# Optimization experiments

Hardware: AMD Instinct MI355X
Metric: run time of the kernel (lower is better)

## Reference

```python
import jax, jax.numpy as jnp
import numpy as np

SEQ, BATCH, HIDDEN = 2048, 2, 1024
NUM_HEADS, HEAD_DIM = 16, 64
LN_EPS = 1e-6
NEG_INF = -1e10


def setup_inputs() -> dict:
    key = jax.random.key(0)
    k1, k2, k3, k4 = jax.random.split(key, 4)
    inputs_q = jax.random.normal(k1, (SEQ, BATCH, HIDDEN), dtype=jnp.float32)
    # mask convention (TE flax): True / 1 => position is masked out
    mask = jax.random.randint(k2, (BATCH, 1, SEQ, SEQ), 0, 2).astype(bool)
    ln_scale = jnp.ones((HIDDEN,), dtype=jnp.float32)
    ln_bias = jnp.zeros((HIDDEN,), dtype=jnp.float32)
    # fused QKV kernel (embed, 3, num_heads*head_dim); query column pre-scaled
    # at init by 1/sqrt(head_dim) (scaled_query_init=True)
    w_qkv = jax.random.normal(k3, (HIDDEN, 3, NUM_HEADS * HEAD_DIM), dtype=jnp.float32) / np.sqrt(HIDDEN)
    w_qkv = w_qkv.at[:, 0, :].divide(np.sqrt(HEAD_DIM))
    w_out = jax.random.normal(k4, (NUM_HEADS * HEAD_DIM, HIDDEN), dtype=jnp.float32) / np.sqrt(NUM_HEADS * HEAD_DIM)
    return {"inputs_q": inputs_q, "mask": mask, "ln_scale": ln_scale,
            "ln_bias": ln_bias, "w_qkv": w_qkv, "w_out": w_out}


def _layernorm(x, scale, bias):
    mean = jnp.mean(x, axis=-1, keepdims=True)
    var = jnp.mean(jnp.square(x - mean), axis=-1, keepdims=True)
    return (x - mean) * jax.lax.rsqrt(var + LN_EPS) * scale + bias


def reference(inputs_q, mask, ln_scale, ln_bias, w_qkv, w_out):
    s, b, e = inputs_q.shape  # (seq, batch, hidden): transpose_batch_sequence=True
    ln_out = _layernorm(inputs_q, ln_scale, ln_bias)
    # fused QKV projection: (s,b,e) @ (e,3,H*D) -> (s,b,3,H*D)
    qkv = jnp.einsum('sbe,ekf->sbkf', ln_out, w_qkv)
    q, k, v = qkv[:, :, 0, :], qkv[:, :, 1, :], qkv[:, :, 2, :]
    q = q.reshape(s, b, NUM_HEADS, HEAD_DIM)
    k = k.reshape(s, b, NUM_HEADS, HEAD_DIM)
    v = v.reshape(s, b, NUM_HEADS, HEAD_DIM)
    # core attention, transpose_batch_sequence layout (seq, batch, h, d)
    logits = jnp.einsum('qbhd,kbhd->bhqk', q, k)
    logits = jnp.where(mask, jnp.asarray(NEG_INF, logits.dtype), logits)
    attn = jax.nn.softmax(logits, axis=-1)
    ctx = jnp.einsum('bhqk,kbhd->qbhd', attn, v).reshape(s, b, NUM_HEADS * HEAD_DIM)
    out = jnp.einsum('sbf,fe->sbe', ctx, w_out)
    return out
```

## Files before the change

### kernel.cpp

```cpp
#include <hip/hip_runtime.h>

typedef __bf16 bf16;
typedef __attribute__((ext_vector_type(8))) __bf16 bf16x8;
typedef __attribute__((ext_vector_type(4))) __bf16 bf16x4;
typedef __attribute__((ext_vector_type(4))) float f32x4;
typedef unsigned long long u64;

static constexpr int S = 2048, B = 2, H = 1024, NH = 16, HD = 64;
static constexpr int ROWS = S * B;
static constexpr int NQKV = 3 * NH * HD;
static constexpr int KBLK = 64;
static constexpr int NT = S / KBLK;
static constexpr int MW = S / 64;
static constexpr float LOG2E = 1.4426950408889634f;

__device__ __forceinline__ int swz(int row, int col) { return col ^ ((row & 7) << 3); }

__device__ __forceinline__ void g2l16(const bf16* g, bf16* l) {
  __builtin_amdgcn_global_load_lds((const __attribute__((address_space(1))) void*)g,
                                   (__attribute__((address_space(3))) void*)l, 16, 0, 0);
}

__global__ __launch_bounds__(256) void prep_kernel(const float* __restrict__ wqkv,
                                                   const float* __restrict__ wout,
                                                   bf16* __restrict__ dqkv,
                                                   bf16* __restrict__ dout,
                                                   const float* __restrict__ x,
                                                   const float* __restrict__ sc,
                                                   const float* __restrict__ bi,
                                                   bf16* __restrict__ lnout,
                                                   const unsigned char* __restrict__ mbytes,
                                                   int* __restrict__ flag) {
  __shared__ float shmem[32 * 33];
  const int bid = blockIdx.x;
  const int tid = threadIdx.x;
  if (bid < 4096) {
    const int bx = bid & 127, by = bid >> 7;
    const bool second = bx >= (NQKV / 32);
    const float* src = second ? wout : wqkv;
    bf16* dst = second ? dout : dqkv;
    const int C = second ? H : NQKV;
    const int c0 = (second ? bx - NQKV / 32 : bx) * 32, r0 = by * 32;
    const int xx = tid & 31, yy = tid >> 5;
#pragma unroll
    for (int i = 0; i < 32; i += 8)
      shmem[(yy + i) * 33 + xx] = src[(size_t)(r0 + yy + i) * C + c0 + xx];
    __syncthreads();
#pragma unroll
    for (int i = 0; i < 32; i += 8) {
      const int col = c0 + yy + i;
      const float scale = (!second && col < 1024) ? LOG2E : 1.0f;
      dst[(size_t)col * H + r0 + xx] = (bf16)(shmem[xx * 33 + yy + i] * scale);
    }
  } else if (bid < 8192) {
    const int row = bid - 4096;
    const float4 v = *(const float4*)&x[(size_t)row * H + tid * 4];
    float s = v.x + v.y + v.z + v.w;
#pragma unroll
    for (int m = 1; m < 64; m <<= 1) s += __shfl_xor(s, m);
    float* red1 = shmem;
    float* red2 = shmem + 8;
    const int w = tid >> 6, lane = tid & 63;
    if (lane == 0) red1[w] = s;
    __syncthreads();
    const float mean = (red1[0] + red1[1] + red1[2] + red1[3]) * (1.0f / H);
    const float dx = v.x - mean, dy = v.y - mean, dz = v.z - mean, dw = v.w - mean;
    float q = dx * dx + dy * dy + dz * dz + dw * dw;
#pragma unroll
    for (int m = 1; m < 64; m <<= 1) q += __shfl_xor(q, m);
    if (lane == 0) red2[w] = q;
    __syncthreads();
    const float var = (red2[0] + red2[1] + red2[2] + red2[3]) * (1.0f / H);
    const float inv = rsqrtf(var + 1e-6f);
    const float4 s4 = *(const float4*)&sc[tid * 4];
    const float4 b4 = *(const float4*)&bi[tid * 4];
    bf16x4 o;
    o[0] = (bf16)(dx * inv * s4.x + b4.x);
    o[1] = (bf16)(dy * inv * s4.y + b4.y);
    o[2] = (bf16)(dz * inv * s4.z + b4.z);
    o[3] = (bf16)(dw * inv * s4.w + b4.w);
    *(bf16x4*)&lnout[(size_t)row * H + tid * 4] = o;
  } else {
    int* cnt = (int*)shmem;
    if (tid == 0) cnt[0] = 0;
    __syncthreads();
    int local = 0;
    for (int i = tid; i < 4096; i += 256)
      if ((i & 3) != 0 && mbytes[i] != 0) local = 1;
    if (local) atomicOr(cnt, 1);
    __syncthreads();
    if (tid == 0) flag[0] = (cnt[0] == 0) ? 1 : 0;
  }
}

__global__ __launch_bounds__(256) void pack_mask(const void* __restrict__ mask, const int* __restrict__ flag,
                                                 u64* __restrict__ bits) {
  const size_t e = (size_t)blockIdx.x * 256 + threadIdx.x;
  int mv;
  if (flag[0] != 0) mv = ((const int*)mask)[e];
  else mv = (int)((const unsigned char*)mask)[e];
  const u64 bal = __ballot(mv != 0);
  if ((threadIdx.x & 63) == 0) bits[e >> 6] = bal;
}

template <int EPI>
__global__ __launch_bounds__(256) void gemm128(const bf16* __restrict__ A, const bf16* __restrict__ Bt,
                                               bf16* __restrict__ qo, bf16* __restrict__ ko,
                                               bf16* __restrict__ vo, float* __restrict__ out) {
  constexpr int K = 1024;
  __shared__ __align__(16) bf16 As[128][64];
  __shared__ __align__(16) bf16 Bs[128][64];
  const int nwg = gridDim.x * gridDim.y;
  const int lin = blockIdx.y * gridDim.x + blockIdx.x;
  const int cpx = nwg >> 3;
  const int work = (lin & 7) * cpx + (lin >> 3);
  const int bm = (work / gridDim.x) * 128, bn = (work % gridDim.x) * 128;
  const int tid = threadIdx.x;
  const int wave = tid >> 6, lane = tid & 63;
  const int wm = (wave >> 1) * 64, wn = (wave & 1) * 64;
  const int g = lane >> 4, l15 = lane & 15;
  const int lr = lane >> 3;
  const int lc = 8 * ((lane & 7) ^ lr);
  f32x4 acc[4][4] = {};
  for (int kt = 0; kt < K; kt += 64) {
#pragma unroll
    for (int p = 0; p < 4; ++p) {
      const int r0 = wave * 32 + p * 8;
      g2l16(&A[(size_t)(bm + r0 + lr) * K + kt + lc], &As[r0][0]);
      g2l16(&Bt[(size_t)(bn + r0 + lr) * K + kt + lc], &Bs[r0][0]);
    }
    __syncthreads();
#pragma unroll
    for (int ks = 0; ks < 2; ++ks) {
      bf16x8 af[4], bb[4];
#pragma unroll
      for (int i = 0; i < 4; ++i) af[i] = *(const bf16x8*)&As[wm + i * 16 + l15][swz(l15, ks * 32 + g * 8)];
#pragma unroll
      for (int j = 0; j < 4; ++j) bb[j] = *(const bf16x8*)&Bs[wn + j * 16 + l15][swz(l15, ks * 32 + g * 8)];
#pragma unroll
      for (int i = 0; i < 4; ++i)
#pragma unroll
        for (int j = 0; j < 4; ++j)
          acc[i][j] = __builtin_amdgcn_mfma_f32_16x16x32_bf16(af[i], bb[j], acc[i][j], 0, 0, 0);
    }
    __syncthreads();
  }
#pragma unroll
  for (int i = 0; i < 4; ++i) {
#pragma unroll
    for (int j = 0; j < 4; ++j) {
#pragma unroll
      for (int r = 0; r < 4; ++r) {
        const int row = bm + wm + i * 16 + g * 4 + r;
        const int col = bn + wn + j * 16 + l15;
        const float val = acc[i][j][r];
        if (EPI == 0) {
          const int kk = col >> 10, f = col & 1023;
          const int h = f >> 6, d = f & 63;
          const int sdx = row >> 1, b = row & 1;
          const size_t head = (size_t)b * NH + h;
          if (kk == 0)
            qo[(head * S + sdx) * HD + d] = (bf16)val;
          else if (kk == 1)
            ko[(head * S + sdx) * HD + d] = (bf16)val;
          else
            vo[(head * HD + d) * S + sdx] = (bf16)val;
        } else {
          out[(size_t)row * H + col] = val;
        }
      }
    }
  }
}

__global__ __launch_bounds__(512, 4) void attn_kernel(const bf16* __restrict__ Qb, const bf16* __restrict__ Kb,
                                                      const bf16* __restrict__ Vt, const u64* __restrict__ mbits,
                                                      bf16* __restrict__ ctx) {
  __shared__ __align__(16) bf16 Ks[2][64][64];
  __shared__ __align__(16) bf16 Vs[2][64][64];
  __shared__ __align__(16) bf16 P[8][16][64];
  const int lin = blockIdx.y * 16 + blockIdx.x;
  const int work = ((lin & 7) << 6) | (lin >> 3);
  const int bh = work >> 4, qb = work & 15;
  const int b = bh >> 4, h = bh & 15;
  const int tid = threadIdx.x, w = tid >> 6, lane = tid & 63;
  const int g = lane >> 4, c = lane & 15;
  const int q0 = qb * 128 + w * 16;
  const size_t head = (size_t)b * NH + h;
  const bf16* Qh = Qb + head * S * HD;
  const bf16* Kh = Kb + head * S * HD;
  const bf16* Vh = Vt + head * HD * S;

  const int srow = w * 8 + (lane >> 3);
  const int scol = 8 * ((lane & 7) ^ (lane >> 3));

  bf16x8 aq[2];
#pragma unroll
  for (int ks = 0; ks < 2; ++ks)
    aq[ks] = *(const bf16x8*)&Qh[(size_t)(q0 + c) * HD + ks * 32 + g * 8];

  f32x4 o[4] = {};
  float lsum = 0.f;

  g2l16(&Kh[(size_t)srow * HD + scol], &Ks[0][w * 8][0]);
  g2l16(&Vh[(size_t)srow * S + scol], &Vs[0][w * 8][0]);
  __syncthreads();

  for (int t = 0; t < NT; ++t) {
    const int cur = t & 1;
    if (t + 1 < NT) {
      const int kt1 = (t + 1) * KBLK;
      g2l16(&Kh[(size_t)(kt1 + srow) * HD + scol], &Ks[cur ^ 1][w * 8][0]);
      g2l16(&Vh[(size_t)srow * S + kt1 + scol], &Vs[cur ^ 1][w * 8][0]);
    }
    f32x4 sv[4] = {};
#pragma unroll
    for (int ks = 0; ks < 2; ++ks) {
      bf16x8 bk[4];
#pragma unroll
      for (int j = 0; j < 4; ++j)
        bk[j] = *(const bf16x8*)&Ks[cur][j * 16 + c][swz(c, ks * 32 + g * 8)];
      __builtin_amdgcn_s_setprio(1);
#pragma unroll
      for (int j = 0; j < 4; ++j)
        sv[j] = __builtin_amdgcn_mfma_f32_16x16x32_bf16(bk[j], aq[ks], sv[j], 0, 0, 0);
      __builtin_amdgcn_s_setprio(0);
    }
    {
      const u64 mb = mbits[((size_t)b * S + q0 + c) * MW + t];
      const unsigned mlo = (unsigned)mb, mhi = (unsigned)(mb >> 32);
      f32x4 acc4 = {0.f, 0.f, 0.f, 0.f};
#pragma unroll
      for (int j = 0; j < 4; ++j) {
        const unsigned word = (j < 2) ? mlo : mhi;
        const unsigned sub = word >> (((j & 1) << 4) + (g << 2));
        bf16x4 pk;
#pragma unroll
        for (int r = 0; r < 4; ++r) {
          float e = __builtin_amdgcn_exp2f(sv[j][r]);
          if ((sub >> r) & 1u) e = 0.f;
          pk[r] = (bf16)e;
          acc4[r] += e;
        }
        *(bf16x4*)&P[w][c][(j * 16 + g * 4) ^ ((c & 7) << 3)] = pk;
      }
      float part = (acc4[0] + acc4[1]) + (acc4[2] + acc4[3]);
      part += __shfl_xor(part, 16);
      part += __shfl_xor(part, 32);
      lsum += part;
    }
    __threadfence_block();
#pragma unroll
    for (int ks = 0; ks < 2; ++ks) {
      const bf16x8 pa = *(const bf16x8*)&P[w][c][(ks * 32 + g * 8) ^ ((c & 7) << 3)];
      bf16x8 bv[4];
#pragma unroll
      for (int j = 0; j < 4; ++j)
        bv[j] = *(const bf16x8*)&Vs[cur][j * 16 + c][swz(c, ks * 32 + g * 8)];
      __builtin_amdgcn_s_setprio(1);
#pragma unroll
      for (int j = 0; j < 4; ++j)
        o[j] = __builtin_amdgcn_mfma_f32_16x16x32_bf16(pa, bv[j], o[j], 0, 0, 0);
      __builtin_amdgcn_s_setprio(0);
    }
    __syncthreads();
  }
#pragma unroll
  for (int r = 0; r < 4; ++r) {
    const float denom = __shfl(lsum, g * 4 + r);
    const float inv = 1.0f / denom;
    const int qrow = q0 + g * 4 + r;
#pragma unroll
    for (int j = 0; j < 4; ++j)
      ctx[((size_t)qrow * B + b) * H + h * HD + j * 16 + c] = (bf16)(o[j][r] * inv);
  }
}

extern "C" void kernel_launch(void* const* d_in, const int* in_sizes, int n_in,
                              void* d_out, int out_size, void* d_ws, size_t ws_size,
                              hipStream_t stream) {
  const float* x = (const float*)d_in[0];
  const void* mask = d_in[1];
  const float* ln_scale = (const float*)d_in[2];
  const float* ln_bias = (const float*)d_in[3];
  const float* w_qkv = (const float*)d_in[4];
  const float* w_out = (const float*)d_in[5];
  float* out = (float*)d_out;

  char* ws = (char*)d_ws;
  size_t off = 0;
  int* flag = (int*)(ws + off); off += 256;
  u64* mbits = (u64*)(ws + off); off += (size_t)B * S * (S / 8);
  bf16* lnb   = (bf16*)(ws + off); off += (size_t)ROWS * H * 2;
  bf16* wqkvt = (bf16*)(ws + off); off += (size_t)NQKV * H * 2;
  bf16* woutt = (bf16*)(ws + off); off += (size_t)H * H * 2;
  bf16* Qb    = (bf16*)(ws + off); off += (size_t)B * NH * S * HD * 2;
  bf16* Kb    = (bf16*)(ws + off); off += (size_t)B * NH * S * HD * 2;
  bf16* Vt    = (bf16*)(ws + off); off += (size_t)B * NH * S * HD * 2;
  bf16* ctx   = (bf16*)(ws + off); off += (size_t)ROWS * H * 2;

  prep_kernel<<<8193, 256, 0, stream>>>(w_qkv, w_out, wqkvt, woutt, x, ln_scale, ln_bias, lnb,
                                        (const unsigned char*)mask, flag);
  pack_mask<<<(B * S * S) / 256, 256, 0, stream>>>(mask, flag, mbits);
  gemm128<0><<<dim3(NQKV / 128, ROWS / 128), 256, 0, stream>>>(lnb, wqkvt, Qb, Kb, Vt, nullptr);
  attn_kernel<<<dim3(S / 128, B * NH), 512, 0, stream>>>(Qb, Kb, Vt, mbits, ctx);
  gemm128<1><<<dim3(H / 128, ROWS / 128), 256, 0, stream>>>(ctx, woutt, nullptr, nullptr, nullptr, out);
}
```

Measured before the change: 164.6 us.

## Switch attention to 32x32 MFMA with register-resident P via lane shuffles

```diff
diff --git a/kernel.cpp b/kernel.cpp
--- a/kernel.cpp
+++ b/kernel.cpp
@@ -3,7 +3,9 @@
 typedef __bf16 bf16;
 typedef __attribute__((ext_vector_type(8))) __bf16 bf16x8;
 typedef __attribute__((ext_vector_type(4))) __bf16 bf16x4;
+typedef __attribute__((ext_vector_type(2))) __bf16 bf16x2;
 typedef __attribute__((ext_vector_type(4))) float f32x4;
+typedef __attribute__((ext_vector_type(16))) float f32x16;
 typedef unsigned long long u64;
 
 static constexpr int S = 2048, B = 2, H = 1024, NH = 16, HD = 64;
@@ -20,6 +22,9 @@
   __builtin_amdgcn_global_load_lds((const __attribute__((address_space(1))) void*)g,
                                    (__attribute__((address_space(3))) void*)l, 16, 0, 0);
 }
+
+union PackU { unsigned u; bf16x2 h; };
+union FragU { unsigned w[4]; bf16x8 v; };
 
 __global__ __launch_bounds__(256) void prep_kernel(const float* __restrict__ wqkv,
                                                    const float* __restrict__ wout,
@@ -173,106 +178,119 @@
   }
 }
 
-__global__ __launch_bounds__(512, 4) void attn_kernel(const bf16* __restrict__ Qb, const bf16* __restrict__ Kb,
+__global__ __launch_bounds__(256, 2) void attn_kernel(const bf16* __restrict__ Qb, const bf16* __restrict__ Kb,
                                                       const bf16* __restrict__ Vt, const u64* __restrict__ mbits,
                                                       bf16* __restrict__ ctx) {
   __shared__ __align__(16) bf16 Ks[2][64][64];
   __shared__ __align__(16) bf16 Vs[2][64][64];
-  __shared__ __align__(16) bf16 P[8][16][64];
   const int lin = blockIdx.y * 16 + blockIdx.x;
   const int work = ((lin & 7) << 6) | (lin >> 3);
   const int bh = work >> 4, qb = work & 15;
   const int b = bh >> 4, h = bh & 15;
   const int tid = threadIdx.x, w = tid >> 6, lane = tid & 63;
-  const int g = lane >> 4, c = lane & 15;
-  const int q0 = qb * 128 + w * 16;
+  const int c32 = lane & 31, hi = lane >> 5;
+  const int q0 = qb * 128 + w * 32;
   const size_t head = (size_t)b * NH + h;
   const bf16* Qh = Qb + head * S * HD;
   const bf16* Kh = Kb + head * S * HD;
   const bf16* Vh = Vt + head * HD * S;
 
-  const int srow = w * 8 + (lane >> 3);
+  const int sra = w * 16 + (lane >> 3);
   const int scol = 8 * ((lane & 7) ^ (lane >> 3));
 
-  bf16x8 aq[2];
-#pragma unroll
-  for (int ks = 0; ks < 2; ++ks)
-    aq[ks] = *(const bf16x8*)&Qh[(size_t)(q0 + c) * HD + ks * 32 + g * 8];
-
-  f32x4 o[4] = {};
-  float lsum = 0.f;
-
-  g2l16(&Kh[(size_t)srow * HD + scol], &Ks[0][w * 8][0]);
-  g2l16(&Vh[(size_t)srow * S + scol], &Vs[0][w * 8][0]);
+  bf16x8 aq[4];
+#pragma unroll
+  for (int s = 0; s < 4; ++s)
+    aq[s] = *(const bf16x8*)&Qh[(size_t)(q0 + c32) * HD + s * 16 + hi * 8];
+
+  f32x16 o[2] = {};
+  f32x4 acc4 = {0.f, 0.f, 0.f, 0.f};
+
+  g2l16(&Kh[(size_t)sra * HD + scol], &Ks[0][w * 16][0]);
+  g2l16(&Kh[(size_t)(sra + 8) * HD + scol], &Ks[0][w * 16 + 8][0]);
+  g2l16(&Vh[(size_t)sra * S + scol], &Vs[0][w * 16][0]);
+  g2l16(&Vh[(size_t)(sra + 8) * S + scol], &Vs[0][w * 16 + 8][0]);
   __syncthreads();
 
   for (int t = 0; t < NT; ++t) {
     const int cur = t & 1;
     if (t + 1 < NT) {
       const int kt1 = (t + 1) * KBLK;
-      g2l16(&Kh[(size_t)(kt1 + srow) * HD + scol], &Ks[cur ^ 1][w * 8][0]);
-      g2l16(&Vh[(size_t)srow * S + kt1 + scol], &Vs[cur ^ 1][w * 8][0]);
-    }
-    f32x4 sv[4] = {};
-#pragma unroll
-    for (int ks = 0; ks < 2; ++ks) {
-      bf16x8 bk[4];
-#pragma unroll
-      for (int j = 0; j < 4; ++j)
-        bk[j] = *(const bf16x8*)&Ks[cur][j * 16 + c][swz(c, ks * 32 + g * 8)];
+      g2l16(&Kh[(size_t)(kt1 + sra) * HD + scol], &Ks[cur ^ 1][w * 16][0]);
+      g2l16(&Kh[(size_t)(kt1 + sra + 8) * HD + scol], &Ks[cur ^ 1][w * 16 + 8][0]);
+      g2l16(&Vh[(size_t)sra * S + kt1 + scol], &Vs[cur ^ 1][w * 16][0]);
+      g2l16(&Vh[(size_t)(sra + 8) * S + kt1 + scol], &Vs[cur ^ 1][w * 16 + 8][0]);
+    }
+    f32x16 sv[2] = {};
+#pragma unroll
+    for (int s = 0; s < 4; ++s) {
+      const bf16x8 bk0 = *(const bf16x8*)&Ks[cur][c32][swz(c32, s * 16 + hi * 8)];
+      const bf16x8 bk1 = *(const bf16x8*)&Ks[cur][32 + c32][swz(c32, s * 16 + hi * 8)];
       __builtin_amdgcn_s_setprio(1);
-#pragma unroll
-      for (int j = 0; j < 4; ++j)
-        sv[j] = __builtin_amdgcn_mfma_f32_16x16x32_bf16(bk[j], aq[ks], sv[j], 0, 0, 0);
+      sv[0] = __builtin_amdgcn_mfma_f32_32x32x16_bf16(bk0, aq[s], sv[0], 0, 0, 0);
+      sv[1] = __builtin_amdgcn_mfma_f32_32x32x16_bf16(bk1, aq[s], sv[1], 0, 0, 0);
       __builtin_amdgcn_s_setprio(0);
     }
+    unsigned PW[2][4][2];
     {
-      const u64 mb = mbits[((size_t)b * S + q0 + c) * MW + t];
-      const unsigned mlo = (unsigned)mb, mhi = (unsigned)(mb >> 32);
-      f32x4 acc4 = {0.f, 0.f, 0.f, 0.f};
-#pragma unroll
-      for (int j = 0; j < 4; ++j) {
-        const unsigned word = (j < 2) ? mlo : mhi;
-        const unsigned sub = word >> (((j & 1) << 4) + (g << 2));
-        bf16x4 pk;
-#pragma unroll
-        for (int r = 0; r < 4; ++r) {
-          float e = __builtin_amdgcn_exp2f(sv[j][r]);
-          if ((sub >> r) & 1u) e = 0.f;
-          pk[r] = (bf16)e;
-          acc4[r] += e;
+      const u64 mb = mbits[((size_t)b * S + q0 + c32) * MW + t];
+      const unsigned m0 = ((unsigned)mb) >> (hi * 4);
+      const unsigned m1 = ((unsigned)(mb >> 32)) >> (hi * 4);
+#pragma unroll
+      for (int j2 = 0; j2 < 2; ++j2) {
+        const unsigned mw = j2 ? m1 : m0;
+#pragma unroll
+        for (int qd = 0; qd < 4; ++qd) {
+          const unsigned bits = mw >> (8 * qd);
+          float e0 = __builtin_amdgcn_exp2f(sv[j2][4 * qd + 0]);
+          float e1 = __builtin_amdgcn_exp2f(sv[j2][4 * qd + 1]);
+          float e2 = __builtin_amdgcn_exp2f(sv[j2][4 * qd + 2]);
+          float e3 = __builtin_amdgcn_exp2f(sv[j2][4 * qd + 3]);
+          if (bits & 1u) e0 = 0.f;
+          if ((bits >> 1) & 1u) e1 = 0.f;
+          if ((bits >> 2) & 1u) e2 = 0.f;
+          if ((bits >> 3) & 1u) e3 = 0.f;
+          acc4[0] += e0; acc4[1] += e1; acc4[2] += e2; acc4[3] += e3;
+          PackU p0, p1;
+          p0.h[0] = (bf16)e0; p0.h[1] = (bf16)e1;
+          p1.h[0] = (bf16)e2; p1.h[1] = (bf16)e3;
+          PW[j2][qd][0] = p0.u;
+          PW[j2][qd][1] = p1.u;
         }
-        *(bf16x4*)&P[w][c][(j * 16 + g * 4) ^ ((c & 7) << 3)] = pk;
       }
-      float part = (acc4[0] + acc4[1]) + (acc4[2] + acc4[3]);
-      part += __shfl_xor(part, 16);
-      part += __shfl_xor(part, 32);
-      lsum += part;
-    }
-    __threadfence_block();
-#pragma unroll
-    for (int ks = 0; ks < 2; ++ks) {
-      const bf16x8 pa = *(const bf16x8*)&P[w][c][(ks * 32 + g * 8) ^ ((c & 7) << 3)];
-      bf16x8 bv[4];
-#pragma unroll
-      for (int j = 0; j < 4; ++j)
-        bv[j] = *(const bf16x8*)&Vs[cur][j * 16 + c][swz(c, ks * 32 + g * 8)];
+    }
+#pragma unroll
+    for (int sp = 0; sp < 4; ++sp) {
+      const int j2 = sp >> 1, s0 = sp & 1;
+      const unsigned a0 = PW[j2][2 * s0][0], a1 = PW[j2][2 * s0][1];
+      const unsigned b0 = PW[j2][2 * s0 + 1][0], b1 = PW[j2][2 * s0 + 1][1];
+      const unsigned snd0 = hi ? a0 : b0, snd1 = hi ? a1 : b1;
+      const unsigned r0 = (unsigned)__shfl_xor((int)snd0, 32);
+      const unsigned r1 = (unsigned)__shfl_xor((int)snd1, 32);
+      FragU pa;
+      pa.w[0] = hi ? r0 : a0;
+      pa.w[1] = hi ? r1 : a1;
+      pa.w[2] = hi ? b0 : r0;
+      pa.w[3] = hi ? b1 : r1;
+      const bf16x8 bv0 = *(const bf16x8*)&Vs[cur][c32][swz(c32, sp * 16 + hi * 8)];
+      const bf16x8 bv1 = *(const bf16x8*)&Vs[cur][32 + c32][swz(c32, sp * 16 + hi * 8)];
       __builtin_amdgcn_s_setprio(1);
-#pragma unroll
-      for (int j = 0; j < 4; ++j)
-        o[j] = __builtin_amdgcn_mfma_f32_16x16x32_bf16(pa, bv[j], o[j], 0, 0, 0);
+      o[0] = __builtin_amdgcn_mfma_f32_32x32x16_bf16(pa.v, bv0, o[0], 0, 0, 0);
+      o[1] = __builtin_amdgcn_mfma_f32_32x32x16_bf16(pa.v, bv1, o[1], 0, 0, 0);
       __builtin_amdgcn_s_setprio(0);
     }
     __syncthreads();
   }
-#pragma unroll
-  for (int r = 0; r < 4; ++r) {
-    const float denom = __shfl(lsum, g * 4 + r);
-    const float inv = 1.0f / denom;
-    const int qrow = q0 + g * 4 + r;
-#pragma unroll
-    for (int j = 0; j < 4; ++j)
-      ctx[((size_t)qrow * B + b) * H + h * HD + j * 16 + c] = (bf16)(o[j][r] * inv);
+  float ls = (acc4[0] + acc4[1]) + (acc4[2] + acc4[3]);
+  ls += __shfl_xor(ls, 32);
+  const float rinv = 1.0f / ls;
+#pragma unroll
+  for (int reg = 0; reg < 16; ++reg) {
+    const int qr = (reg & 3) + 8 * (reg >> 2) + 4 * hi;
+    const float iv = __shfl(rinv, qr);
+    const int qrow = q0 + qr;
+    ctx[((size_t)qrow * B + b) * H + h * HD + c32] = (bf16)(o[0][reg] * iv);
+    ctx[((size_t)qrow * B + b) * H + h * HD + 32 + c32] = (bf16)(o[1][reg] * iv);
   }
 }
 
@@ -303,6 +321,6 @@
                                         (const unsigned char*)mask, flag);
   pack_mask<<<(B * S * S) / 256, 256, 0, stream>>>(mask, flag, mbits);
   gemm128<0><<<dim3(NQKV / 128, ROWS / 128), 256, 0, stream>>>(lnb, wqkvt, Qb, Kb, Vt, nullptr);
-  attn_kernel<<<dim3(S / 128, B * NH), 512, 0, stream>>>(Qb, Kb, Vt, mbits, ctx);
+  attn_kernel<<<dim3(S / 128, B * NH), 256, 0, stream>>>(Qb, Kb, Vt, mbits, ctx);
   gemm128<1><<<dim3(H / 128, ROWS / 128), 256, 0, stream>>>(ctx, woutt, nullptr, nullptr, nullptr, out);
 }
```

After: 169.7 us. +3.1%, slower.
